# Optimization experiments

Hardware: AMD Instinct MI355X
Metric: run time of the kernel (lower is better)

The kernel has to match this reference:

```python
import jax, jax.numpy as jnp
from jax import lax
import numpy as np

B, MAX_FRAME, CAPLEN = 64, 40, 20
H, E, V = 512, 512, 32000


def setup_inputs() -> dict:
    key = jax.random.key(0)
    ks = jax.random.split(key, 9)
    s = 0.02
    return {
        "feature": jax.random.normal(ks[0], (B, MAX_FRAME + CAPLEN, H), dtype=jnp.float32),
        "captions": jax.random.randint(ks[1], (B, CAPLEN), 0, V),
        "embedding": jax.random.normal(ks[2], (V, E), dtype=jnp.float32) * s,
        "W_ih": jax.random.normal(ks[3], (4 * H, E + H), dtype=jnp.float32) * s,
        "W_hh": jax.random.normal(ks[4], (4 * H, H), dtype=jnp.float32) * s,
        "b_ih": jax.random.normal(ks[5], (4 * H,), dtype=jnp.float32) * s,
        "b_hh": jax.random.normal(ks[6], (4 * H,), dtype=jnp.float32) * s,
        "W_lin": jax.random.normal(ks[7], (V, H), dtype=jnp.float32) * s,
        "b_lin": jax.random.normal(ks[8], (V,), dtype=jnp.float32) * s,
    }


def _lstm_scan(xs, W_ih, W_hh, b, h0, c0):
    """xs: [T, B, D]; PyTorch gate order i, f, g, o."""
    def step(carry, x):
        h, c = carry
        gates = x @ W_ih.T + h @ W_hh.T + b  # [B, 4H]
        i, f, g, o = jnp.split(gates, 4, axis=-1)
        c = jax.nn.sigmoid(f) * c + jax.nn.sigmoid(i) * jnp.tanh(g)
        h = jax.nn.sigmoid(o) * jnp.tanh(c)
        return (h, c), h
    _, hs = lax.scan(step, (h0, c0), xs)
    return hs  # [T, B, H]


def reference(feature, captions, embedding, W_ih, W_hh, b_ih, b_hh, W_lin, b_lin):
    batch = feature.shape[0]
    caplen = captions.shape[1]
    max_frame = feature.shape[1] - caplen
    hdim = W_hh.shape[1]
    edim = embedding.shape[1]

    emb = embedding[captions]  # [B, caplen, E]
    # encoding phase: pad token (zeros) concat frame feature
    pad = jnp.zeros((batch, max_frame, edim), feature.dtype)
    enc_x = jnp.concatenate([pad, feature[:, :max_frame, :]], axis=2)  # [B, mf, E+H]
    # decoding phase: embedded word concat frame feature
    dec_x = jnp.concatenate([emb, feature[:, max_frame:, :]], axis=2)  # [B, caplen, E+H]
    xs = jnp.concatenate([enc_x, dec_x], axis=1).transpose(1, 0, 2)  # [T, B, E+H]

    h0 = jnp.zeros((batch, hdim), feature.dtype)
    c0 = jnp.zeros((batch, hdim), feature.dtype)
    hs = _lstm_scan(xs, W_ih, W_hh, b_ih + b_hh, h0, c0)  # [T, B, H]

    dec_h = hs[max_frame:].transpose(1, 0, 2)  # [B, caplen, H]
    logits = dec_h @ W_lin.T + b_lin  # [B, caplen, V]
    logits = logits[:, :-1, :]  # drop last step, as in original
    return logits.reshape(batch * (caplen - 1), -1)
```

## Files before the change

kernel.cpp:

```cpp
#include <hip/hip_runtime.h>
#include <hip/hip_bf16.h>


typedef short bf16x8 __attribute__((ext_vector_type(8)));
typedef float f32x4 __attribute__((ext_vector_type(4)));

__device__ inline short f2bf(float f) {
    unsigned u = __float_as_uint(f);
    unsigned r = (u + 0x7fffu + ((u >> 16) & 1u)) >> 16;
    return (short)r;
}
__device__ inline int4 ld8_f32_to_bf16(const float* __restrict__ g) {
    float4 a = *(const float4*)g;
    float4 b = *(const float4*)(g + 4);
    union { short s[8]; int4 v; } u;
    u.s[0] = f2bf(a.x); u.s[1] = f2bf(a.y); u.s[2] = f2bf(a.z); u.s[3] = f2bf(a.w);
    u.s[4] = f2bf(b.x); u.s[5] = f2bf(b.y); u.s[6] = f2bf(b.z); u.s[7] = f2bf(b.w);
    return u.v;
}
__device__ inline float sig_fast(float x) {
    return __builtin_amdgcn_rcpf(1.0f + __expf(-x));
}
__device__ inline float tanh_fast(float x) {
    return 1.0f - 2.0f * __builtin_amdgcn_rcpf(1.0f + __expf(2.0f * x));
}
__device__ inline void gload_lds16(const void* g, void* l) {
    __builtin_amdgcn_global_load_lds(
        (const __attribute__((address_space(1))) void*)g,
        (__attribute__((address_space(3))) void*)l, 16, 0, 0);
}

#define LSTM_BLOCKS 32

__global__ __launch_bounds__(256) void prep_new(
    const float* __restrict__ feature,
    const int*   __restrict__ captions,
    const float* __restrict__ embedding,
    const float* __restrict__ W_ih,
    const float* __restrict__ W_lin,
    short* __restrict__ xs,
    short* __restrict__ wih,
    short* __restrict__ wbf,
    unsigned* __restrict__ flags)
{
    const int tid = threadIdx.x;
    if (blockIdx.x == 0 && tid < 64) flags[tid] = 0;

    const int NF = 3840 * 64;
    const int NE = 1280 * 64;
    const int NW = 2048 * 128;
    const int NL = 2048000;
    const int total = NF + NE + NW + NL;
    const int stride = gridDim.x * 256;

    for (int idx = blockIdx.x * 256 + tid; idx < total; idx += stride) {
        if (idx < NF) {
            int row = idx >> 6, c8 = (idx & 63) * 8;
            int t = row >> 6, b = row & 63;
            *(int4*)&xs[(size_t)row * 1024 + 512 + c8] =
                ld8_f32_to_bf16(&feature[(size_t)(b * 60 + t) * 512 + c8]);
        } else if (idx < NF + NE) {
            int j = idx - NF;
            int r = j >> 6, c8 = (j & 63) * 8;
            int t = 40 + (r >> 6), b = r & 63;
            int tok = captions[b * 20 + (t - 40)];
            *(int4*)&xs[(size_t)(2560 + r) * 1024 + c8] =
                ld8_f32_to_bf16(&embedding[(size_t)tok * 512 + c8]);
        } else if (idx < NF + NE + NW) {
            int j = idx - NF - NE;
            *(int4*)&wih[(size_t)j * 8] = ld8_f32_to_bf16(&W_ih[(size_t)j * 8]);
        } else {
            int j = idx - NF - NE - NW;
            *(int4*)&wbf[(size_t)j * 8] = ld8_f32_to_bf16(&W_lin[(size_t)j * 8]);
        }
    }
}

__global__ __launch_bounds__(256) void xproj_gemm(
    const short* __restrict__ xs,
    const short* __restrict__ wih,
    const float* __restrict__ b_ih,
    const float* __restrict__ b_hh,
    float* __restrict__ Xp)
{
    __shared__ __align__(16) short Al[128 * 64];
    __shared__ __align__(16) short Bl[128 * 64];
    const int tid  = threadIdx.x;
    const int wave = tid >> 6, lane = tid & 63;
    const int quad = lane >> 4, l16 = lane & 15;
    const int m0 = blockIdx.y * 128;
    const int n0 = blockIdx.x * 128;
    const int wm = (wave >> 1) * 64, wn = (wave & 1) * 64;
    const int kstart = (blockIdx.y >= 20) ? 0 : 512;

    const char* Ab = (const char*)xs;
    const char* Wb = (const char*)wih;
    char* AlB = (char*)Al;
    char* BlB = (char*)Bl;

    f32x4 acc[4][4] = {};

    for (int k0 = kstart; k0 < 1024; k0 += 64) {
#pragma unroll
        for (int p = 0; p < 4; ++p) {
            int row = p * 32 + wave * 8 + (lane >> 3);
            int ss  = ((lane & 7) ^ (row & 7)) << 4;
            gload_lds16(Ab + (size_t)(m0 + row) * 2048 + k0 * 2 + ss,
                        AlB + p * 4096 + wave * 1024);
            gload_lds16(Wb + (size_t)(n0 + row) * 2048 + k0 * 2 + ss,
                        BlB + p * 4096 + wave * 1024);
        }
        __syncthreads();
#pragma unroll
        for (int kk = 0; kk < 64; kk += 32) {
            bf16x8 af[4], bg[4];
            const int s_ = (kk >> 3) + quad;
#pragma unroll
            for (int i = 0; i < 4; ++i) {
                int rw = wm + i * 16 + l16;
                af[i] = *(const bf16x8*)&Al[rw * 64 + ((s_ ^ (rw & 7)) << 3)];
            }
#pragma unroll
            for (int jj = 0; jj < 4; ++jj) {
                int rw = wn + jj * 16 + l16;
                bg[jj] = *(const bf16x8*)&Bl[rw * 64 + ((s_ ^ (rw & 7)) << 3)];
            }
#pragma unroll
            for (int i = 0; i < 4; ++i)
#pragma unroll
                for (int jj = 0; jj < 4; ++jj)
                    acc[i][jj] = __builtin_amdgcn_mfma_f32_16x16x32_bf16(
                        af[i], bg[jj], acc[i][jj], 0, 0, 0);
        }
        __syncthreads();
    }

#pragma unroll
    for (int jj = 0; jj < 4; ++jj) {
        int n = n0 + wn + jj * 16 + l16;
        float bv = b_ih[n] + b_hh[n];
#pragma unroll
        for (int i = 0; i < 4; ++i) {
            int mbase = m0 + wm + i * 16 + quad * 4;
#pragma unroll
            for (int r = 0; r < 4; ++r)
                Xp[(size_t)(mbase + r) * 2048 + n] = acc[i][jj][r] + bv;
        }
    }
}

__global__ __launch_bounds__(256) void prep_old(
    const float* __restrict__ feature,
    const int*   __restrict__ captions,
    const float* __restrict__ embedding,
    const float* __restrict__ W_ih,
    const float* __restrict__ b_ih,
    const float* __restrict__ b_hh,
    float* __restrict__ Xp,
    const float* __restrict__ W_lin,
    short* __restrict__ wbf,
    unsigned* __restrict__ flags)
{
    const int blk = blockIdx.x;
    const int tid = threadIdx.x;

    if (blk == 480) {
        if (tid < 64) flags[tid] = 0;
        return;
    }
    if (blk > 480) {
        if (wbf) {
            int i = (blk - 481) * 256 + tid;
            if (i < 2048000)
                *(int4*)&wbf[(size_t)i * 8] = ld8_f32_to_bf16(&W_lin[(size_t)i * 8]);
        }
        return;
    }

    __shared__ __align__(16) short Al[128 * 72];
    __shared__ __align__(16) short Bl[128 * 72];
    const int wave = tid >> 6, lane = tid & 63;
    const int quad = lane >> 4, l16 = lane & 15;
    const int bx = blk & 15, by = blk >> 4;
    const int m0 = by * 128;
    const int n0 = bx * 128;
    const int wm = (wave >> 1) * 64, wn = (wave & 1) * 64;
    const int sr = tid >> 3;
    const int sc = (tid & 7) * 8;
    const bool dec = (by >= 20);
    const int kstart = dec ? 0 : 512;

    f32x4 acc[4][4] = {};

    for (int k0 = kstart; k0 < 1024; k0 += 64) {
        const int j = k0 + sc;
#pragma unroll
        for (int p = 0; p < 4; ++p) {
            int r = sr + p * 32;
            int row = m0 + r;
            int t = row >> 6, b = row & 63;
            int4 val;
            if (dec && j < 512) {
                int tok = captions[b * 20 + (t - 40)];
                val = ld8_f32_to_bf16(&embedding[(size_t)tok * 512 + j]);
            } else {
                val = ld8_f32_to_bf16(&feature[(size_t)(b * 60 + t) * 512 + (j - 512)]);
            }
            *(int4*)&Al[r * 72 + sc] = val;
            *(int4*)&Bl[r * 72 + sc] = ld8_f32_to_bf16(&W_ih[(size_t)(n0 + r) * 1024 + j]);
        }
        __syncthreads();
#pragma unroll
        for (int kk = 0; kk < 64; kk += 32) {
            bf16x8 af[4], bg[4];
#pragma unroll
            for (int i = 0; i < 4; ++i)
                af[i] = *(const bf16x8*)&Al[(wm + i * 16 + l16) * 72 + kk + quad * 8];
#pragma unroll
            for (int jj = 0; jj < 4; ++jj)
                bg[jj] = *(const bf16x8*)&Bl[(wn + jj * 16 + l16) * 72 + kk + quad * 8];
#pragma unroll
            for (int i = 0; i < 4; ++i)
#pragma unroll
                for (int jj = 0; jj < 4; ++jj)
                    acc[i][jj] = __builtin_amdgcn_mfma_f32_16x16x32_bf16(
                        af[i], bg[jj], acc[i][jj], 0, 0, 0);
        }
        __syncthreads();
    }

#pragma unroll
    for (int jj = 0; jj < 4; ++jj) {
        int n = n0 + wn + jj * 16 + l16;
        float bv = b_ih[n] + b_hh[n];
#pragma unroll
        for (int i = 0; i < 4; ++i) {
            int mbase = m0 + wm + i * 16 + quad * 4;
#pragma unroll
            for (int r = 0; r < 4; ++r)
                Xp[(size_t)(mbase + r) * 2048 + n] = acc[i][jj][r] + bv;
        }
    }
}

template <bool BF16B>
__global__ __launch_bounds__(256) void gemm_out(
    const short* __restrict__ A,
    const void*  __restrict__ Wv,
    const float* __restrict__ bias,
    float* __restrict__ C,
    int M, int N, int K)
{
    __shared__ __align__(16) short Al[128 * 72];
    __shared__ __align__(16) short Bl[128 * 72];
    const int tid  = threadIdx.x;
    const int wave = tid >> 6, lane = tid & 63;
    const int quad = lane >> 4, l16 = lane & 15;
    const int m0 = blockIdx.y * 128;
    const int n0 = blockIdx.x * 128;
    const int wm = (wave >> 1) * 64, wn = (wave & 1) * 64;
    const int sr = tid >> 3;
    const int sc = (tid & 7) * 8;

    f32x4 acc[4][4] = {};

    for (int k0 = 0; k0 < K; k0 += 64) {
        if (BF16B) {
            const char* Ab = (const char*)A;
            const char* Wb = (const char*)Wv;
            char* AlB = (char*)Al;
            char* BlB = (char*)Bl;
#pragma unroll
            for (int p = 0; p < 4; ++p) {
                int row = p * 32 + wave * 8 + (lane >> 3);
                int ss  = ((lane & 7) ^ (row & 7)) << 4;
                int am  = m0 + row; am = (am < M) ? am : (M - 1);
                gload_lds16(Ab + (size_t)am * 1024 + k0 * 2 + ss,
                            AlB + p * 4096 + wave * 1024);
                gload_lds16(Wb + (size_t)(n0 + row) * 1024 + k0 * 2 + ss,
                            BlB + p * 4096 + wave * 1024);
            }
        } else {
#pragma unroll
            for (int p = 0; p < 4; ++p) {
                int r = sr + p * 32;
                int am = m0 + r;
                am = (am < M) ? am : (M - 1);
                *(int4*)&Al[r * 72 + sc] = *(const int4*)&A[(size_t)am * K + k0 + sc];
                *(int4*)&Bl[r * 72 + sc] =
                    ld8_f32_to_bf16(&((const float*)Wv)[(size_t)(n0 + r) * K + k0 + sc]);
            }
        }
        __syncthreads();
#pragma unroll
        for (int kk = 0; kk < 64; kk += 32) {
            bf16x8 af[4], bg[4];
            if (BF16B) {
                const int s_ = (kk >> 3) + quad;
#pragma unroll
                for (int i = 0; i < 4; ++i) {
                    int rw = wm + i * 16 + l16;
                    af[i] = *(const bf16x8*)&Al[rw * 64 + ((s_ ^ (rw & 7)) << 3)];
                }
#pragma unroll
                for (int jj = 0; jj < 4; ++jj) {
                    int rw = wn + jj * 16 + l16;
                    bg[jj] = *(const bf16x8*)&Bl[rw * 64 + ((s_ ^ (rw & 7)) << 3)];
                }
            } else {
#pragma unroll
                for (int i = 0; i < 4; ++i)
                    af[i] = *(const bf16x8*)&Al[(wm + i * 16 + l16) * 72 + kk + quad * 8];
#pragma unroll
                for (int jj = 0; jj < 4; ++jj)
                    bg[jj] = *(const bf16x8*)&Bl[(wn + jj * 16 + l16) * 72 + kk + quad * 8];
            }
#pragma unroll
            for (int i = 0; i < 4; ++i)
#pragma unroll
                for (int jj = 0; jj < 4; ++jj)
                    acc[i][jj] = __builtin_amdgcn_mfma_f32_16x16x32_bf16(
                        af[i], bg[jj], acc[i][jj], 0, 0, 0);
        }
        __syncthreads();
    }

#pragma unroll
    for (int jj = 0; jj < 4; ++jj) {
        int n = n0 + wn + jj * 16 + l16;
        float bv = bias[n];
#pragma unroll
        for (int i = 0; i < 4; ++i) {
            int mbase = m0 + wm + i * 16 + quad * 4;
#pragma unroll
            for (int r = 0; r < 4; ++r) {
                int ar = mbase + r;
                if (ar < M) {
                    int crow = (ar & 63) * 19 + (ar >> 6);
                    C[(size_t)crow * N + n] = acc[i][jj][r] + bv;
                }
            }
        }
    }
}

__global__ __launch_bounds__(256, 1) void mega(
    const float* __restrict__ Xp,
    const float* __restrict__ W_hh,
    unsigned long long* __restrict__ hbuf,
    unsigned long long* __restrict__ dec_h,
    unsigned* __restrict__ flags,
    const short* __restrict__ wbf,
    const float* __restrict__ b_lin,
    float* __restrict__ out)
{
    __shared__ __align__(16) char smem[67584];
    const int tid  = threadIdx.x;
    const int wave = tid >> 6, lane = tid & 63;
    const int quad = lane >> 4, l16 = lane & 15;

    if (blockIdx.x < LSTM_BLOCKS) {
        short* Wl  = (short*)smem;
        short* Htb = (short*)(smem + 65536);
        const int nb = blockIdx.x * 16;
        const int swz = (l16 & 7) << 3;

#pragma unroll
        for (int it = 0; it < 16; ++it) {
            int rr = (tid >> 6) + it * 4;
            int k  = (tid & 63) * 8;
            int s = rr >> 4, col = rr & 15;
            *(int4*)&Wl[(rr * 512 + k) ^ ((rr & 7) << 3)] =
                ld8_f32_to_bf16(&W_hh[(size_t)(s * 512 + nb + col) * 512 + k]);
        }
        float creg[4] = {0.f, 0.f, 0.f, 0.f};

        const int n = nb + l16;
        float xg[4][4];
#pragma unroll
        for (int r = 0; r < 4; ++r) {
            const float* xr = Xp + (size_t)(wave * 16 + quad * 4 + r) * 2048;
            xg[r][0] = xr[n];
            xg[r][1] = xr[512 + n];
            xg[r][2] = xr[1024 + n];
            xg[r][3] = xr[1536 + n];
        }
        __syncthreads();

        for (int t = 0; t < 59; ++t) {
            f32x4 acc[4] = {};
            if (t > 0) {
                const unsigned long long* hrow =
                    hbuf + ((size_t)((t & 1) ^ 1) << 13)
                         + (size_t)(wave * 16 + l16) * 128 + quad * 2;
                union { unsigned long long q[2]; bf16x8 v; } hu[16];
#pragma unroll
                for (int kk = 0; kk < 16; ++kk) {
                    hu[kk].q[0] = __hip_atomic_load(&hrow[kk * 8],
                                     __ATOMIC_RELAXED, __HIP_MEMORY_SCOPE_AGENT);
                    hu[kk].q[1] = __hip_atomic_load(&hrow[kk * 8 + 1],
                                     __ATOMIC_RELAXED, __HIP_MEMORY_SCOPE_AGENT);
                }
                __builtin_amdgcn_sched_barrier(0);
#pragma unroll
                for (int kk = 0; kk < 16; ++kk) {
#pragma unroll
                    for (int s = 0; s < 4; ++s) {
                        bf16x8 bg = *(const bf16x8*)
                            &Wl[((s * 16 + l16) * 512 + kk * 32 + quad * 8) ^ swz];
                        acc[s] = __builtin_amdgcn_mfma_f32_16x16x32_bf16(
                            hu[kk].v, bg, acc[s], 0, 0, 0);
                    }
                }
            }
#pragma unroll
            for (int r = 0; r < 4; ++r) {
                float iv = acc[0][r] + xg[r][0];
                float fv = acc[1][r] + xg[r][1];
                float gv = acc[2][r] + xg[r][2];
                float ov = acc[3][r] + xg[r][3];
                float cn = sig_fast(fv) * creg[r] + sig_fast(iv) * tanh_fast(gv);
                float hn = sig_fast(ov) * tanh_fast(cn);
                creg[r] = cn;
                Htb[(wave << 8) + ((quad * 4 + r) << 4) + l16] = f2bf(hn);
            }
            asm volatile("s_waitcnt lgkmcnt(0)" ::: "memory");
            unsigned long long* hout64 = hbuf + ((size_t)(t & 1) << 13);
            {
                int row = lane >> 2, qp = lane & 3;
                unsigned long long v =
                    *(const unsigned long long*)&Htb[(wave << 8) + (row << 4) + qp * 4];
                int m = wave * 16 + row;
                __hip_atomic_store(&hout64[m * 128 + (nb >> 2) + qp], v,
                                   __ATOMIC_RELAXED, __HIP_MEMORY_SCOPE_AGENT);
                if (t >= 40)
                    __hip_atomic_store(
                        &dec_h[(size_t)((t - 40) * 64 + m) * 128 + (nb >> 2) + qp], v,
                        __ATOMIC_RELAXED, __HIP_MEMORY_SCOPE_AGENT);
            }
            if (t < 58) {
                float xn_[4][4];
                const float* xt = Xp + (size_t)(t + 1) * 131072;
#pragma unroll
                for (int r = 0; r < 4; ++r) {
                    const float* xr = xt + (size_t)(wave * 16 + quad * 4 + r) * 2048;
                    xn_[r][0] = xr[n];
                    xn_[r][1] = xr[512 + n];
                    xn_[r][2] = xr[1024 + n];
                    xn_[r][3] = xr[1536 + n];
                }
                __syncthreads();
                if (tid == 0)
                    __hip_atomic_store(&flags[blockIdx.x], (unsigned)(t + 1),
                                       __ATOMIC_RELAXED, __HIP_MEMORY_SCOPE_AGENT);
                if (tid < LSTM_BLOCKS) {
                    int guard = 0;
                    while (__hip_atomic_load(&flags[tid], __ATOMIC_RELAXED,
                                             __HIP_MEMORY_SCOPE_AGENT) < (unsigned)(t + 1)
                           && guard < (1 << 16)) {
                        __builtin_amdgcn_s_sleep(1);
                        ++guard;
                    }
                }
                __syncthreads();
                if (blockIdx.x == 0 && tid == 0)
                    __hip_atomic_store(&flags[32], (unsigned)(t + 1),
                                       __ATOMIC_RELAXED, __HIP_MEMORY_SCOPE_AGENT);
#pragma unroll
                for (int r = 0; r < 4; ++r)
#pragma unroll
                    for (int g = 0; g < 4; ++g)
                        xg[r][g] = xn_[r][g];
            }
        }
        __syncthreads();
        if (tid == 0)
            __hip_atomic_store(&flags[blockIdx.x], 59u,
                               __ATOMIC_RELAXED, __HIP_MEMORY_SCOPE_AGENT);
        if (blockIdx.x == 0) {
            if (tid < LSTM_BLOCKS) {
                int guard = 0;
                while (__hip_atomic_load(&flags[tid], __ATOMIC_RELAXED,
                                         __HIP_MEMORY_SCOPE_AGENT) < 59u
                       && guard < (1 << 16)) {
                    __builtin_amdgcn_s_sleep(1);
                    ++guard;
                }
            }
            __syncthreads();
            if (tid == 0)
                __hip_atomic_store(&flags[32], 59u,
                                   __ATOMIC_RELAXED, __HIP_MEMORY_SCOPE_AGENT);
        }
        return;
    }

    short* Al = (short*)smem;
    short* Bl = (short*)(smem + 18432);
    const int cid = blockIdx.x - LSTM_BLOCKS;
    const int n0 = (cid % 250) * 128;
    const int mt = cid / 250;
    const int m0 = mt * 128;
    const int M = 1216;
    const int wm = (wave >> 1) * 64, wn = (wave & 1) * 64;
    const int sr = tid >> 3;
    const int sc = (tid & 7) * 8;
    int maxa = m0 + 127; maxa = (maxa < M - 1) ? maxa : (M - 1);
    const unsigned v = 41u + (unsigned)(maxa >> 6);

    if (tid == 0) {
        int guard = 0;
        while (__hip_atomic_load(&flags[32], __ATOMIC_RELAXED,
                                 __HIP_MEMORY_SCOPE_AGENT) < v
               && guard < (1 << 14)) {
            __builtin_amdgcn_s_sleep(64);
            ++guard;
        }
    }
    __syncthreads();

    f32x4 acc[4][4] = {};
    const char* Wb = (const char*)wbf;
    char* BlB = (char*)Bl;

    for (int k0 = 0; k0 < 512; k0 += 64) {
#pragma unroll
        for (int p = 0; p < 4; ++p) {
            int r = sr + p * 32;
            int ar = m0 + r; ar = (ar < M) ? ar : (M - 1);
            size_t qi = (size_t)ar * 128 + ((k0 + sc) >> 2);
            union { unsigned long long q[2]; int4 v4; } u;
            u.q[0] = __hip_atomic_load(&dec_h[qi],
                         __ATOMIC_RELAXED, __HIP_MEMORY_SCOPE_AGENT);
            u.q[1] = __hip_atomic_load(&dec_h[qi + 1],
                         __ATOMIC_RELAXED, __HIP_MEMORY_SCOPE_AGENT);
            *(int4*)&Al[r * 72 + sc] = u.v4;
        }
#pragma unroll
        for (int p = 0; p < 4; ++p) {
            int row = p * 32 + wave * 8 + (lane >> 3);
            int ss  = ((lane & 7) ^ (row & 7)) << 4;
            gload_lds16(Wb + (size_t)(n0 + row) * 1024 + k0 * 2 + ss,
                        BlB + p * 4096 + wave * 1024);
        }
        __syncthreads();
#pragma unroll
        for (int kk = 0; kk < 64; kk += 32) {
            bf16x8 af[4], bg[4];
            const int s_ = (kk >> 3) + quad;
#pragma unroll
            for (int i = 0; i < 4; ++i)
                af[i] = *(const bf16x8*)&Al[(wm + i * 16 + l16) * 72 + kk + quad * 8];
#pragma unroll
            for (int jj = 0; jj < 4; ++jj) {
                int rw = wn + jj * 16 + l16;
                bg[jj] = *(const bf16x8*)&Bl[rw * 64 + ((s_ ^ (rw & 7)) << 3)];
            }
#pragma unroll
            for (int i = 0; i < 4; ++i)
#pragma unroll
                for (int jj = 0; jj < 4; ++jj)
                    acc[i][jj] = __builtin_amdgcn_mfma_f32_16x16x32_bf16(
                        af[i], bg[jj], acc[i][jj], 0, 0, 0);
        }
        __syncthreads();
    }

#pragma unroll
    for (int jj = 0; jj < 4; ++jj) {
        int n = n0 + wn + jj * 16 + l16;
        float bv = b_lin[n];
#pragma unroll
        for (int i = 0; i < 4; ++i) {
            int mbase = m0 + wm + i * 16 + quad * 4;
#pragma unroll
            for (int r = 0; r < 4; ++r) {
                int ar = mbase + r;
                if (ar < M) {
                    int crow = (ar & 63) * 19 + (ar >> 6);
                    out[(size_t)crow * 32000 + n] = acc[i][jj][r] + bv;
                }
            }
        }
    }
}

extern "C" void kernel_launch(void* const* d_in, const int* in_sizes, int n_in,
                              void* d_out, int out_size, void* d_ws, size_t ws_size,
                              hipStream_t stream)
{
    (void)in_sizes; (void)n_in; (void)out_size;
    const float* feature   = (const float*)d_in[0];
    const int*   captions  = (const int*)d_in[1];
    const float* embedding = (const float*)d_in[2];
    const float* W_ih      = (const float*)d_in[3];
    const float* W_hh      = (const float*)d_in[4];
    const float* b_ih      = (const float*)d_in[5];
    const float* b_hh      = (const float*)d_in[6];
    const float* W_lin     = (const float*)d_in[7];
    const float* b_lin     = (const float*)d_in[8];
    float* out = (float*)d_out;

    char* ws = (char*)d_ws;
    unsigned long long* hbuf = (unsigned long long*)(ws);
    unsigned long long* dech = (unsigned long long*)(ws + 131072);
    unsigned* flags = (unsigned*)(ws + 1376256);
    short*    wbf   = (short*)(ws + 1376512);
    float*    xpws  = (float*)(ws + 34144512);
    const bool big  = ws_size >= (size_t)34144512;
    const bool bigx = ws_size >= (size_t)34144512 + 31457280;

    if (bigx) {
        short* xs  = (short*)((char*)d_out + 143589376);
        short* wih = (short*)((char*)d_out + 151453696);
        float* Xp  = xpws;

        prep_new<<<2048, 256, 0, stream>>>(
            feature, captions, embedding, W_ih, W_lin, xs, wih, wbf, flags);

        xproj_gemm<<<dim3(16, 30), 256, 0, stream>>>(xs, wih, b_ih, b_hh, Xp);

        mega<<<dim3(LSTM_BLOCKS + 2500), 256, 0, stream>>>(
            Xp, W_hh, hbuf, dech, flags, wbf, b_lin, out);
    } else {
        float* Xp = (float*)d_out;
        prep_old<<<dim3(big ? 8481 : 481), 256, 0, stream>>>(
            feature, captions, embedding, W_ih, b_ih, b_hh, Xp,
            W_lin, big ? wbf : (short*)nullptr, flags);
        mega<<<dim3(LSTM_BLOCKS), 256, 0, stream>>>(
            Xp, W_hh, hbuf, dech, flags, (const short*)nullptr, b_lin, out);
        if (big)
            gemm_out<true><<<dim3(250, 10), 256, 0, stream>>>(
                (const short*)dech, wbf, b_lin, out, 1216, 32000, 512);
        else
            gemm_out<false><<<dim3(250, 10), 256, 0, stream>>>(
                (const short*)dech, W_lin, b_lin, out, 1216, 32000, 512);
    }
}
```

Baseline: 674.7 us.

## Launch one prep thread per element, drop swizzled async GEMM load path, enlarge flags

The prep kernel switches from a grid-stride loop over 2048 blocks to one thread per 8-element chunk with a 10304-block launch. The BF16B gemm_out path drops its direct global-to-LDS async loads and XOR-swizzled layout and uses the padded register-staged copy instead. The flag array grows to 128 entries and the workspace offsets shift to match. The swizzle removal looks like a simplification or revert that may lower GEMM load efficiency. The larger flag clear hints that the LSTM sync scheme changed in code not shown.

```diff
diff --git a/kernel.cpp b/kernel.cpp
--- a/kernel.cpp
+++ b/kernel.cpp
@@ -44,35 +44,32 @@
     unsigned* __restrict__ flags)
 {
     const int tid = threadIdx.x;
-    if (blockIdx.x == 0 && tid < 64) flags[tid] = 0;
+    if (blockIdx.x == 0 && tid < 128) flags[tid] = 0;
 
     const int NF = 3840 * 64;
     const int NE = 1280 * 64;
     const int NW = 2048 * 128;
     const int NL = 2048000;
-    const int total = NF + NE + NW + NL;
-    const int stride = gridDim.x * 256;
-
-    for (int idx = blockIdx.x * 256 + tid; idx < total; idx += stride) {
-        if (idx < NF) {
-            int row = idx >> 6, c8 = (idx & 63) * 8;
-            int t = row >> 6, b = row & 63;
-            *(int4*)&xs[(size_t)row * 1024 + 512 + c8] =
-                ld8_f32_to_bf16(&feature[(size_t)(b * 60 + t) * 512 + c8]);
-        } else if (idx < NF + NE) {
-            int j = idx - NF;
-            int r = j >> 6, c8 = (j & 63) * 8;
-            int t = 40 + (r >> 6), b = r & 63;
-            int tok = captions[b * 20 + (t - 40)];
-            *(int4*)&xs[(size_t)(2560 + r) * 1024 + c8] =
-                ld8_f32_to_bf16(&embedding[(size_t)tok * 512 + c8]);
-        } else if (idx < NF + NE + NW) {
-            int j = idx - NF - NE;
-            *(int4*)&wih[(size_t)j * 8] = ld8_f32_to_bf16(&W_ih[(size_t)j * 8]);
-        } else {
-            int j = idx - NF - NE - NW;
-            *(int4*)&wbf[(size_t)j * 8] = ld8_f32_to_bf16(&W_lin[(size_t)j * 8]);
-        }
+    const int idx = blockIdx.x * 256 + tid;
+
+    if (idx < NF) {
+        int row = idx >> 6, c8 = (idx & 63) * 8;
+        int t = row >> 6, b = row & 63;
+        *(int4*)&xs[(size_t)row * 1024 + 512 + c8] =
+            ld8_f32_to_bf16(&feature[(size_t)(b * 60 + t) * 512 + c8]);
+    } else if (idx < NF + NE) {
+        int j = idx - NF;
+        int r = j >> 6, c8 = (j & 63) * 8;
+        int t = 40 + (r >> 6), b = r & 63;
+        int tok = captions[b * 20 + (t - 40)];
+        *(int4*)&xs[(size_t)(2560 + r) * 1024 + c8] =
+            ld8_f32_to_bf16(&embedding[(size_t)tok * 512 + c8]);
+    } else if (idx < NF + NE + NW) {
+        int j = idx - NF - NE;
+        *(int4*)&wih[(size_t)j * 8] = ld8_f32_to_bf16(&W_ih[(size_t)j * 8]);
+    } else if (idx < NF + NE + NW + NL) {
+        int j = idx - NF - NE - NW;
+        *(int4*)&wbf[(size_t)j * 8] = ld8_f32_to_bf16(&W_lin[(size_t)j * 8]);
     }
 }
 
@@ -165,7 +162,7 @@
     const int tid = threadIdx.x;
 
     if (blk == 480) {
-        if (tid < 64) flags[tid] = 0;
+        if (tid < 128) flags[tid] = 0;
         return;
     }
     if (blk > 480) {
@@ -265,56 +262,29 @@
     f32x4 acc[4][4] = {};
 
     for (int k0 = 0; k0 < K; k0 += 64) {
-        if (BF16B) {
-            const char* Ab = (const char*)A;
-            const char* Wb = (const char*)Wv;
-            char* AlB = (char*)Al;
-            char* BlB = (char*)Bl;
-#pragma unroll
-            for (int p = 0; p < 4; ++p) {
-                int row = p * 32 + wave * 8 + (lane >> 3);
-                int ss  = ((lane & 7) ^ (row & 7)) << 4;
-                int am  = m0 + row; am = (am < M) ? am : (M - 1);
-                gload_lds16(Ab + (size_t)am * 1024 + k0 * 2 + ss,
-                            AlB + p * 4096 + wave * 1024);
-                gload_lds16(Wb + (size_t)(n0 + row) * 1024 + k0 * 2 + ss,
-                            BlB + p * 4096 + wave * 1024);
-            }
-        } else {
-#pragma unroll
-            for (int p = 0; p < 4; ++p) {
-                int r = sr + p * 32;
-                int am = m0 + r;
-                am = (am < M) ? am : (M - 1);
-                *(int4*)&Al[r * 72 + sc] = *(const int4*)&A[(size_t)am * K + k0 + sc];
+#pragma unroll
+        for (int p = 0; p < 4; ++p) {
+            int r = sr + p * 32;
+            int am = m0 + r;
+            am = (am < M) ? am : (M - 1);
+            *(int4*)&Al[r * 72 + sc] = *(const int4*)&A[(size_t)am * K + k0 + sc];
+            if (BF16B)
+                *(int4*)&Bl[r * 72 + sc] =
+                    *(const int4*)&((const short*)Wv)[(size_t)(n0 + r) * K + k0 + sc];
+            else
                 *(int4*)&Bl[r * 72 + sc] =
                     ld8_f32_to_bf16(&((const float*)Wv)[(size_t)(n0 + r) * K + k0 + sc]);
-            }
         }
         __syncthreads();
 #pragma unroll
         for (int kk = 0; kk < 64; kk += 32) {
             bf16x8 af[4], bg[4];
-            if (BF16B) {
-                const int s_ = (kk >> 3) + quad;
-#pragma unroll
-                for (int i = 0; i < 4; ++i) {
-                    int rw = wm + i * 16 + l16;
-                    af[i] = *(const bf16x8*)&Al[rw * 64 + ((s_ ^ (rw & 7)) << 3)];
-                }
-#pragma unroll
-                for (int jj = 0; jj < 4; ++jj) {
-                    int rw = wn + jj * 16 + l16;
-                    bg[jj] = *(const bf16x8*)&Bl[rw * 64 + ((s_ ^ (rw & 7)) << 3)];
-                }
-            } else {
-#pragma unroll
-                for (int i = 0; i < 4; ++i)
-                    af[i] = *(const bf16x8*)&Al[(wm + i * 16 + l16) * 72 + kk + quad * 8];
-#pragma unroll
-                for (int jj = 0; jj < 4; ++jj)
-                    bg[jj] = *(const bf16x8*)&Bl[(wn + jj * 16 + l16) * 72 + kk + quad * 8];
-            }
+#pragma unroll
+            for (int i = 0; i < 4; ++i)
+                af[i] = *(const bf16x8*)&Al[(wm + i * 16 + l16) * 72 + kk + quad * 8];
+#pragma unroll
+            for (int jj = 0; jj < 4; ++jj)
+                bg[jj] = *(const bf16x8*)&Bl[(wn + jj * 16 + l16) * 72 + kk + quad * 8];
 #pragma unroll
             for (int i = 0; i < 4; ++i)
 #pragma unroll
@@ -605,17 +575,17 @@
     unsigned long long* hbuf = (unsigned long long*)(ws);
     unsigned long long* dech = (unsigned long long*)(ws + 131072);
     unsigned* flags = (unsigned*)(ws + 1376256);
-    short*    wbf   = (short*)(ws + 1376512);
-    float*    xpws  = (float*)(ws + 34144512);
-    const bool big  = ws_size >= (size_t)34144512;
-    const bool bigx = ws_size >= (size_t)34144512 + 31457280;
+    short*    wbf   = (short*)(ws + 1376768);
+    float*    xpws  = (float*)(ws + 34144768);
+    const bool big  = ws_size >= (size_t)34144768;
+    const bool bigx = ws_size >= (size_t)34144768 + 31457280;
 
     if (bigx) {
         short* xs  = (short*)((char*)d_out + 143589376);
         short* wih = (short*)((char*)d_out + 151453696);
         float* Xp  = xpws;
 
-        prep_new<<<2048, 256, 0, stream>>>(
+        prep_new<<<10304, 256, 0, stream>>>(
             feature, captions, embedding, W_ih, W_lin, xs, wih, wbf, flags);
 
         xproj_gemm<<<dim3(16, 30), 256, 0, stream>>>(xs, wih, b_ih, b_hh, Xp);
```

Result: no change. 672.5 us (-0.3%).
